# Kernel optimization log

Measured on AMD Instinct MI355X. Metric: run time of the kernel, lower is better.

Reference implementation:

```python
import jax, jax.numpy as jnp
import numpy as np

EPS = 1e-08

def setup_inputs() -> dict:
    key = jax.random.key(0)
    x = jax.random.normal(key, (16, 2048), dtype=jnp.float32)  # [B, L]
    return {"x": x}

def reference(x) -> jnp.ndarray:
    # min-max normalize per series to [-1, 1]
    min_x = jnp.min(x, axis=1, keepdims=True)
    max_x = jnp.max(x, axis=1, keepdims=True)
    scaled = 2.0 * ((x - min_x) / (max_x - min_x + EPS)) - 1.0
    scaled = jnp.clip(scaled, -1.0 + EPS, 1.0 - EPS)
    phi = jnp.arccos(scaled)                      # [B, L]
    gaf = jnp.cos(phi[:, :, None] + phi[:, None, :])  # [B, L, L]
    return gaf
```

## Files before the change

kernel.cpp:

```cpp
#include <hip/hip_runtime.h>
#include <hip/hip_bf16.h>
#include <math.h>

#define L 2048
#define NB 16
#define ROWS_PER_BLOCK 16
#define THREADS 256
#define GAF_EPS 1e-8f

__global__ __launch_bounds__(THREADS) void gaf_kernel(const float* __restrict__ x,
                                                      float* __restrict__ out) {
    __shared__ float sc[L];
    __shared__ float ss[L];
    __shared__ float red[8];

    const int chunks_per_batch = L / ROWS_PER_BLOCK;
    const int b = blockIdx.x / chunks_per_batch;
    const int i0 = (blockIdx.x % chunks_per_batch) * ROWS_PER_BLOCK;
    const int t = threadIdx.x;
    const float* __restrict__ xrow = x + (size_t)b * L;

    float v[8];
    float mn = INFINITY, mx = -INFINITY;
#pragma unroll
    for (int k = 0; k < 8; ++k) {
        v[k] = xrow[t + k * THREADS];
        mn = fminf(mn, v[k]);
        mx = fmaxf(mx, v[k]);
    }
#pragma unroll
    for (int off = 32; off > 0; off >>= 1) {
        mn = fminf(mn, __shfl_down(mn, off));
        mx = fmaxf(mx, __shfl_down(mx, off));
    }
    const int wave = t >> 6;
    if ((t & 63) == 0) { red[wave] = mn; red[4 + wave] = mx; }
    __syncthreads();
    if (t == 0) {
        red[0] = fminf(fminf(red[0], red[1]), fminf(red[2], red[3]));
        red[4] = fmaxf(fmaxf(red[4], red[5]), fmaxf(red[6], red[7]));
    }
    __syncthreads();
    mn = red[0];
    mx = red[4];
    const float inv = 1.0f / (mx - mn + GAF_EPS);

#pragma unroll
    for (int k = 0; k < 8; ++k) {
        float c = 2.0f * ((v[k] - mn) * inv) - 1.0f;
        c = fminf(fmaxf(c, -1.0f + GAF_EPS), 1.0f - GAF_EPS);
        const int idx = t + k * THREADS;
        sc[idx] = c;
        ss[idx] = sqrtf(fmaxf(1.0f - c * c, 0.0f));
    }
    __syncthreads();

    float* __restrict__ obase = out + ((size_t)b * L + (size_t)i0) * L;
#pragma unroll
    for (int i = 0; i < ROWS_PER_BLOCK; ++i) {
        const float ci = sc[i0 + i];
        const float si = ss[i0 + i];
        float4* __restrict__ orow = (float4*)(obase + (size_t)i * L);
#pragma unroll
        for (int it = 0; it < L / (4 * THREADS); ++it) {
            const int j4 = t + it * THREADS;
            const float4 cj = ((const float4*)sc)[j4];
            const float4 sj = ((const float4*)ss)[j4];
            float4 o;
            o.x = ci * cj.x - si * sj.x;
            o.y = ci * cj.y - si * sj.y;
            o.z = ci * cj.z - si * sj.z;
            o.w = ci * cj.w - si * sj.w;
            orow[j4] = o;
        }
    }
}

extern "C" void kernel_launch(void* const* d_in, const int* in_sizes, int n_in,
                              void* d_out, int out_size, void* d_ws, size_t ws_size,
                              hipStream_t stream) {
    const float* x = (const float*)d_in[0];
    float* out = (float*)d_out;
    const dim3 grid(NB * (L / ROWS_PER_BLOCK));
    gaf_kernel<<<grid, THREADS, 0, stream>>>(x, out);
}
```

Before: 253.9 us.

## Use nontemporal stores, hoist row coefficients, and drop a reduction barrier

The output writes now use nontemporal vector stores, so the 256 MB result streams past the caches instead of polluting them. The loops are swapped so each column chunk of cos and sin values is read from LDS once and reused across all 16 rows, with the row coefficients kept in registers. The min/max reduction uses xor shuffles, and every thread reads the per-wave partials directly, which removes one __syncthreads. The kernel is bound by write bandwidth, so the store hint is the main lever, at the cost of more register pressure from the hoisted arrays.

```diff
diff --git a/kernel.cpp b/kernel.cpp
--- a/kernel.cpp
+++ b/kernel.cpp
@@ -1,5 +1,4 @@
 #include <hip/hip_runtime.h>
-#include <hip/hip_bf16.h>
 #include <math.h>
 
 #define L 2048
@@ -7,6 +6,8 @@
 #define ROWS_PER_BLOCK 16
 #define THREADS 256
 #define GAF_EPS 1e-8f
+
+typedef float f32x4 __attribute__((ext_vector_type(4)));
 
 __global__ __launch_bounds__(THREADS) void gaf_kernel(const float* __restrict__ x,
                                                       float* __restrict__ out) {
@@ -30,19 +31,14 @@
     }
 #pragma unroll
     for (int off = 32; off > 0; off >>= 1) {
-        mn = fminf(mn, __shfl_down(mn, off));
-        mx = fmaxf(mx, __shfl_down(mx, off));
+        mn = fminf(mn, __shfl_xor(mn, off));
+        mx = fmaxf(mx, __shfl_xor(mx, off));
     }
     const int wave = t >> 6;
     if ((t & 63) == 0) { red[wave] = mn; red[4 + wave] = mx; }
     __syncthreads();
-    if (t == 0) {
-        red[0] = fminf(fminf(red[0], red[1]), fminf(red[2], red[3]));
-        red[4] = fmaxf(fmaxf(red[4], red[5]), fmaxf(red[6], red[7]));
-    }
-    __syncthreads();
-    mn = red[0];
-    mx = red[4];
+    mn = fminf(fminf(red[0], red[1]), fminf(red[2], red[3]));
+    mx = fmaxf(fmaxf(red[4], red[5]), fmaxf(red[6], red[7]));
     const float inv = 1.0f / (mx - mn + GAF_EPS);
 
 #pragma unroll
@@ -55,23 +51,27 @@
     }
     __syncthreads();
 
+    float ci[ROWS_PER_BLOCK], si[ROWS_PER_BLOCK];
+#pragma unroll
+    for (int i = 0; i < ROWS_PER_BLOCK; ++i) {
+        ci[i] = sc[i0 + i];
+        si[i] = ss[i0 + i];
+    }
+
     float* __restrict__ obase = out + ((size_t)b * L + (size_t)i0) * L;
 #pragma unroll
-    for (int i = 0; i < ROWS_PER_BLOCK; ++i) {
-        const float ci = sc[i0 + i];
-        const float si = ss[i0 + i];
-        float4* __restrict__ orow = (float4*)(obase + (size_t)i * L);
+    for (int it = 0; it < L / (4 * THREADS); ++it) {
+        const int j4 = t + it * THREADS;
+        const f32x4 cj = ((const f32x4*)sc)[j4];
+        const f32x4 sj = ((const f32x4*)ss)[j4];
 #pragma unroll
-        for (int it = 0; it < L / (4 * THREADS); ++it) {
-            const int j4 = t + it * THREADS;
-            const float4 cj = ((const float4*)sc)[j4];
-            const float4 sj = ((const float4*)ss)[j4];
-            float4 o;
-            o.x = ci * cj.x - si * sj.x;
-            o.y = ci * cj.y - si * sj.y;
-            o.z = ci * cj.z - si * sj.z;
-            o.w = ci * cj.w - si * sj.w;
-            orow[j4] = o;
+        for (int i = 0; i < ROWS_PER_BLOCK; ++i) {
+            f32x4 o;
+            o.x = ci[i] * cj.x - si[i] * sj.x;
+            o.y = ci[i] * cj.y - si[i] * sj.y;
+            o.z = ci[i] * cj.z - si[i] * sj.z;
+            o.w = ci[i] * cj.w - si[i] * sj.w;
+            __builtin_nontemporal_store(o, (f32x4*)(obase + (size_t)i * L) + j4);
         }
     }
 }
```

Result: slower. 262.3 us (+3.3%).
